# Performance work log

Measured on AMD Instinct MI355X. Metric: run time of the kernel, lower is better.

The kernel has to match this reference:

```python
import jax, jax.numpy as jnp
import numpy as np

N, K = 16384, 32          # num bboxes, context size
IN_F, HID = 608, 384      # in_features, hidden_dim
ALPHA = 0.2               # LeakyReLU slope
NEG_INF = -9e15


def setup_inputs() -> dict:
    key = jax.random.key(0)
    k1, k2, k3, k4, k5, k6, k7, k8 = jax.random.split(key, 8)
    h_i = jax.random.normal(k1, (N, IN_F), dtype=jnp.float32)
    idx = jax.random.randint(k2, (N, K), 0, N)
    pad = jax.random.uniform(k3, (N, K)) < 0.2
    context_indices = jnp.where(pad, -1, idx).astype(jnp.int64)
    s_in = 1.0 / np.sqrt(IN_F)
    s_a = 1.0 / np.sqrt(2 * HID)
    W_i = jax.random.uniform(k4, (IN_F, HID), minval=-s_in, maxval=s_in, dtype=jnp.float32)
    W_j = jax.random.uniform(k5, (IN_F, HID), minval=-s_in, maxval=s_in, dtype=jnp.float32)
    a_i = jax.random.uniform(k6, (HID,), minval=-s_a, maxval=s_a, dtype=jnp.float32)
    a_j = jax.random.uniform(k7, (HID,), minval=-s_a, maxval=s_a, dtype=jnp.float32)
    a_b = jax.random.uniform(k8, (1,), minval=-s_a, maxval=s_a, dtype=jnp.float32)
    return {"h_i": h_i, "context_indices": context_indices,
            "W_i": W_i, "W_j": W_j, "a_i": a_i, "a_j": a_j, "a_b": a_b}


def reference(h_i, context_indices, W_i, W_j, a_i, a_j, a_b):
    n = h_i.shape[0]
    Wh_i = h_i @ W_i                          # [N, H]
    # W_j has no bias, so projecting then gathering (zero pad row) equals
    # gathering zero-padded features then projecting.
    Wh_all = h_i @ W_j                        # [N, H]
    Wh_pad = jnp.concatenate([Wh_all, jnp.zeros((1, HID), Wh_all.dtype)], axis=0)
    idx = jnp.where(context_indices >= 0, context_indices, n)   # -1 -> zero row
    Wh_j = Wh_pad[idx]                        # [N, K, H] gather
    # attention_layer(concat(Wh_i, Wh_j)) == Wh_i@a_i + Wh_j@a_j + b
    scores = (Wh_i @ a_i)[:, None] + Wh_j @ a_j + a_b[0]        # [N, K]
    scores = jnp.where(scores > 0, scores, ALPHA * scores)      # LeakyReLU
    scores = jnp.where(context_indices >= 0, scores, NEG_INF)   # mask padding
    att = jax.nn.softmax(scores, axis=1)                        # [N, K]
    h_prime = jnp.einsum('nk,nkh->nh', att, Wh_j)               # [N, H]
    return h_prime
```

## Files before the change

kernel.cpp:

```cpp
#include <hip/hip_runtime.h>
#include <hip/hip_bf16.h>

typedef unsigned short u16;
typedef unsigned int u32;
typedef __attribute__((ext_vector_type(8))) __bf16 bf16x8;
typedef __attribute__((ext_vector_type(4))) float f32x4;

#define KCTX 32
#define INF_ 608
#define HID_ 384

#define WH_OFF 0
#define BT_OFF 12582912
#define V_OFF  13049856
#define SI_OFF 13052288
#define SJ_OFF 13117824
#define FL_OFF 13183360

__device__ __forceinline__ float bfu(u16 u)  { return __uint_as_float(((u32)u) << 16); }
__device__ __forceinline__ float bflo(u32 u) { return __uint_as_float(u << 16); }
__device__ __forceinline__ float bfhi(u32 u) { return __uint_as_float(u & 0xffff0000u); }
__device__ __forceinline__ u16 f2bf(float x) {
  u32 u = __float_as_uint(x);
  return (u16)((u + 0x7fffu + ((u >> 16) & 1u)) >> 16);
}
__device__ __forceinline__ void async_ld16(const void* g, void* l) {
  __builtin_amdgcn_global_load_lds(
      (const __attribute__((address_space(1))) u32*)g,
      (__attribute__((address_space(3))) u32*)l, 16, 0, 0);
}

__global__ __launch_bounds__(64) void detect_kernel(
    const u32* __restrict__ hw, const int* __restrict__ ci, int* __restrict__ flags) {
  const int lane = threadIdx.x;
  const u32 w = hw[lane];
  const int e = (int)((w >> 7) & 0xffu);
  const int bad = (e > 134 || e < 100) ? 1 : 0;
  const unsigned long long mb = __ballot(bad);
  const int hi = ci[2 * lane + 1];
  const int z = (hi == 0 || hi == -1) ? 1 : 0;
  const unsigned long long mz = __ballot(z);
  if (lane == 0) {
    flags[0] = (__popcll(mb) >= 16) ? 1 : 0;
    flags[1] = (__popcll(mz) >= 48) ? 1 : 0;
  }
}

__global__ __launch_bounds__(256) void prep_kernel(
    const void* __restrict__ Wi, const void* __restrict__ Wj,
    const void* __restrict__ ai, u16* __restrict__ Bt, float* __restrict__ v,
    const int* __restrict__ flags) {
  const int f32m = flags[0];
  const int t = blockIdx.x * 256 + threadIdx.x;
  const int hh = t / INF_;
  const int ff = t - hh * INF_;
  Bt[t] = f32m ? f2bf(((const float*)Wj)[ff * HID_ + hh])
               : ((const u16*)Wj)[ff * HID_ + hh];
  if (t < INF_) {
    float s = 0.f;
    if (f32m) {
      const float* wi = (const float*)Wi + (size_t)t * HID_;
      const float* a  = (const float*)ai;
      for (int c = 0; c < HID_; ++c) s += wi[c] * a[c];
    } else {
      const u16* wi = (const u16*)Wi + (size_t)t * HID_;
      const u16* a  = (const u16*)ai;
      for (int c = 0; c < HID_; ++c) s += bfu(wi[c]) * bfu(a[c]);
    }
    v[t] = s;
  }
}

__global__ __launch_bounds__(256, 2) void gemm_kernel(
    const void* __restrict__ A, const u16* __restrict__ Bt,
    u16* __restrict__ C, const int* __restrict__ flags) {
  __shared__ __align__(16) u16 As[128][32];
  __shared__ __align__(16) u16 Bs[128][32];
  const int f32m = flags[0];
  const int tid  = threadIdx.x;
  const int lane = tid & 63;
  const int wave = tid >> 6;
  const int row0 = blockIdx.x * 128;
  const int col0 = blockIdx.y * 128;
  const int wm = (wave & 1) * 64;
  const int wn = (wave >> 1) * 64;

  f32x4 acc[4][4];
#pragma unroll
  for (int i = 0; i < 4; ++i)
#pragma unroll
    for (int j = 0; j < 4; ++j) acc[i][j] = (f32x4){0.f, 0.f, 0.f, 0.f};

  const int c0 = tid, c1 = tid + 256;
  const int rA0 = c0 >> 2, kc0 = (c0 & 3) * 16;
  const int rA1 = c1 >> 2, kc1 = (c1 & 3) * 16;
  const char* Ab  = (const char*)A;
  const char* Btb = (const char*)Bt;

  for (int kt = 0; kt < 19; ++kt) {
    const size_t kb = (size_t)kt * 64;
    if (!f32m) {
      async_ld16(Ab + (size_t)(row0 + rA0) * 1216 + kb + kc0, (char*)As + c0 * 16);
      async_ld16(Ab + (size_t)(row0 + rA1) * 1216 + kb + kc1, (char*)As + c1 * 16);
    } else {
      const float* Af = (const float*)A;
#pragma unroll
      for (int j = 0; j < 4; ++j) {
        const int c = tid + j * 256;
        const int r = c >> 3, q = c & 7;
        const float4 fv = *(const float4*)(Af + (size_t)(row0 + r) * INF_ + kt * 32 + q * 4);
        ushort4 sv;
        sv.x = f2bf(fv.x); sv.y = f2bf(fv.y); sv.z = f2bf(fv.z); sv.w = f2bf(fv.w);
        *(ushort4*)&As[r][q * 4] = sv;
      }
    }
    async_ld16(Btb + (size_t)(col0 + rA0) * 1216 + kb + kc0, (char*)Bs + c0 * 16);
    async_ld16(Btb + (size_t)(col0 + rA1) * 1216 + kb + kc1, (char*)Bs + c1 * 16);
    __syncthreads();

    const int kk = (lane >> 4) * 8;
    const int lm = lane & 15;
    bf16x8 af[4], bfr[4];
#pragma unroll
    for (int i = 0; i < 4; ++i) af[i]  = *(const bf16x8*)&As[wm + i * 16 + lm][kk];
#pragma unroll
    for (int i = 0; i < 4; ++i) bfr[i] = *(const bf16x8*)&Bs[wn + i * 16 + lm][kk];
#pragma unroll
    for (int im = 0; im < 4; ++im)
#pragma unroll
      for (int in = 0; in < 4; ++in)
        acc[im][in] = __builtin_amdgcn_mfma_f32_16x16x32_bf16(
            af[im], bfr[in], acc[im][in], 0, 0, 0);
    __syncthreads();
  }

  const int lm = lane & 15, lq = lane >> 4;
#pragma unroll
  for (int im = 0; im < 4; ++im)
#pragma unroll
    for (int in = 0; in < 4; ++in) {
      const int colg = col0 + wn + in * 16 + lm;
#pragma unroll
      for (int r = 0; r < 4; ++r) {
        const int rowg = row0 + wm + im * 16 + lq * 4 + r;
        C[(size_t)rowg * HID_ + colg] = f2bf(acc[im][in][r]);
      }
    }
}

__global__ __launch_bounds__(256) void si_kernel(
    const void* __restrict__ h, const float* __restrict__ v,
    float* __restrict__ si, const int* __restrict__ flags) {
  const int f32m = flags[0];
  const int wave = threadIdx.x >> 6, lane = threadIdx.x & 63;
  const int n = blockIdx.x * 4 + wave;
  float sum = 0.f;
  if (f32m) {
    const float4* row = (const float4*)((const float*)h + (size_t)n * INF_);
    for (int c = lane; c < 152; c += 64) {
      float4 u = row[c];
      const float* vp = v + c * 4;
      sum += u.x * vp[0] + u.y * vp[1] + u.z * vp[2] + u.w * vp[3];
    }
  } else {
    const uint4* row = (const uint4*)((const u16*)h + (size_t)n * INF_);
    for (int c = lane; c < 76; c += 64) {
      uint4 u = row[c];
      const float* vp = v + c * 8;
      sum += bflo(u.x) * vp[0] + bfhi(u.x) * vp[1]
           + bflo(u.y) * vp[2] + bfhi(u.y) * vp[3]
           + bflo(u.z) * vp[4] + bfhi(u.z) * vp[5]
           + bflo(u.w) * vp[6] + bfhi(u.w) * vp[7];
    }
  }
#pragma unroll
  for (int o = 32; o; o >>= 1) sum += __shfl_down(sum, o);
  if (lane == 0) si[n] = sum;
}

__global__ __launch_bounds__(256) void sj_kernel(
    const u16* __restrict__ Wh, const void* __restrict__ aj,
    float* __restrict__ sj, const int* __restrict__ flags) {
  const int f32m = flags[0];
  const int wave = threadIdx.x >> 6, lane = threadIdx.x & 63;
  const int n = blockIdx.x * 4 + wave;
  const uint4* row = (const uint4*)(Wh + (size_t)n * HID_);
  float sum = 0.f;
  for (int c = lane; c < 48; c += 64) {
    uint4 u = row[c];
    float a0, a1, a2, a3, a4, a5, a6, a7;
    if (f32m) {
      const float* af = (const float*)aj + c * 8;
      a0 = af[0]; a1 = af[1]; a2 = af[2]; a3 = af[3];
      a4 = af[4]; a5 = af[5]; a6 = af[6]; a7 = af[7];
    } else {
      uint4 av = ((const uint4*)aj)[c];
      a0 = bflo(av.x); a1 = bfhi(av.x); a2 = bflo(av.y); a3 = bfhi(av.y);
      a4 = bflo(av.z); a5 = bfhi(av.z); a6 = bflo(av.w); a7 = bfhi(av.w);
    }
    sum += bflo(u.x) * a0 + bfhi(u.x) * a1 + bflo(u.y) * a2 + bfhi(u.y) * a3
         + bflo(u.z) * a4 + bfhi(u.z) * a5 + bflo(u.w) * a6 + bfhi(u.w) * a7;
  }
#pragma unroll
  for (int o = 32; o; o >>= 1) sum += __shfl_down(sum, o);
  if (lane == 0) sj[n] = sum;
}

__global__ __launch_bounds__(256) void attn_kernel(
    const int* __restrict__ ci, const float* __restrict__ si,
    const float* __restrict__ sj, const void* __restrict__ ab,
    const u16* __restrict__ Wh, void* __restrict__ out,
    const int* __restrict__ flags) {
  const int f32m = flags[0], i64 = flags[1];
  __shared__ float att_s[2][32];
  __shared__ int   idx_s[2][32];
  const int sub = threadIdx.x & 127;
  const int rb  = threadIdx.x >> 7;
  const int n   = blockIdx.x * 2 + rb;

  if (sub < 32) {
    const size_t t = (size_t)n * KCTX + sub;
    int idx;
    if (i64) { int lo = ci[2 * t], hi2 = ci[2 * t + 1]; idx = (hi2 < 0) ? -1 : lo; }
    else     { idx = ci[t]; }
    const bool valid = idx >= 0;
    const float sjv = valid ? sj[idx] : 0.f;
    const float bias = f32m ? ((const float*)ab)[0] : bfu(((const u16*)ab)[0]);
    float raw = si[n] + sjv + bias;
    float lr = raw > 0.f ? raw : 0.2f * raw;
    float s = valid ? lr : -9e15f;
    float m = s;
#pragma unroll
    for (int o = 16; o; o >>= 1) m = fmaxf(m, __shfl_xor(m, o));
    float p = expf(s - m);
    float d = p;
#pragma unroll
    for (int o = 16; o; o >>= 1) d += __shfl_xor(d, o);
    att_s[rb][sub] = valid ? p / d : 0.f;
    idx_s[rb][sub] = valid ? idx : 0;
  }
  __syncthreads();

  float a0 = 0.f, a1 = 0.f, a2 = 0.f;
#pragma unroll 4
  for (int k = 0; k < KCTX; ++k) {
    const float w = att_s[rb][k];
    const u16* row = Wh + (size_t)idx_s[rb][k] * HID_;
    a0 += w * bfu(row[sub]);
    a1 += w * bfu(row[sub + 128]);
    a2 += w * bfu(row[sub + 256]);
  }
  const size_t ob = (size_t)n * HID_;
  if (f32m) {
    float* o = (float*)out;
    o[ob + sub] = a0; o[ob + sub + 128] = a1; o[ob + sub + 256] = a2;
  } else {
    u16* o = (u16*)out;
    o[ob + sub] = f2bf(a0); o[ob + sub + 128] = f2bf(a1); o[ob + sub + 256] = f2bf(a2);
  }
}

extern "C" void kernel_launch(void* const* d_in, const int* in_sizes, int n_in,
                              void* d_out, int out_size, void* d_ws, size_t ws_size,
                              hipStream_t stream) {
  const void* h  = d_in[0];
  const int*  ci = (const int*)d_in[1];
  const void* Wi = d_in[2];
  const void* Wj = d_in[3];
  const void* ai = d_in[4];
  const void* aj = d_in[5];
  const void* ab = d_in[6];

  char* ws = (char*)d_ws;
  u16*   Wh = (u16*)(ws + WH_OFF);
  u16*   Bt = (u16*)(ws + BT_OFF);
  float* v  = (float*)(ws + V_OFF);
  float* si = (float*)(ws + SI_OFF);
  float* sj = (float*)(ws + SJ_OFF);
  int*   fl = (int*)(ws + FL_OFF);

  detect_kernel<<<1, 64, 0, stream>>>((const u32*)h, ci, fl);
  prep_kernel<<<912, 256, 0, stream>>>(Wi, Wj, ai, Bt, v, fl);
  dim3 g(128, 3);
  gemm_kernel<<<g, 256, 0, stream>>>(h, Bt, Wh, fl);
  si_kernel<<<4096, 256, 0, stream>>>(h, v, si, fl);
  sj_kernel<<<4096, 256, 0, stream>>>(Wh, aj, sj, fl);
  attn_kernel<<<8192, 256, 0, stream>>>(ci, si, sj, ab, Wh, d_out, fl);
}
```

Before: 185.1 us.

## Fuse detect/si/sj kernels into prep, GEMM epilogue and attention kernel

Removes the separate detect, si and sj kernels. Dtype detection is now done inline in each kernel. The s_j dot product is computed in the GEMM epilogue through shuffle reductions and atomicAdd, and s_i is computed inside the attention kernel. The prep kernel transposes W_j through a shared-memory tile and also zeroes sj. Attention now uses one wave per row with 16-byte gathers and __expf. This cuts three launches and the extra passes over Wh and h, at the cost of atomics and nondeterministic summation order in sj.

```diff
diff --git a/kernel.cpp b/kernel.cpp
--- a/kernel.cpp
+++ b/kernel.cpp
@@ -13,9 +13,7 @@
 #define WH_OFF 0
 #define BT_OFF 12582912
 #define V_OFF  13049856
-#define SI_OFF 13052288
-#define SJ_OFF 13117824
-#define FL_OFF 13183360
+#define SJ_OFF 13052288
 
 __device__ __forceinline__ float bfu(u16 u)  { return __uint_as_float(((u32)u) << 16); }
 __device__ __forceinline__ float bflo(u32 u) { return __uint_as_float(u << 16); }
@@ -30,53 +28,80 @@
       (__attribute__((address_space(3))) u32*)l, 16, 0, 0);
 }
 
-__global__ __launch_bounds__(64) void detect_kernel(
-    const u32* __restrict__ hw, const int* __restrict__ ci, int* __restrict__ flags) {
-  const int lane = threadIdx.x;
-  const u32 w = hw[lane];
+__device__ __forceinline__ int detect_f32(const u32* hw) {
+  const u32 w = hw[threadIdx.x & 63];
   const int e = (int)((w >> 7) & 0xffu);
-  const int bad = (e > 134 || e < 100) ? 1 : 0;
-  const unsigned long long mb = __ballot(bad);
-  const int hi = ci[2 * lane + 1];
-  const int z = (hi == 0 || hi == -1) ? 1 : 0;
-  const unsigned long long mz = __ballot(z);
-  if (lane == 0) {
-    flags[0] = (__popcll(mb) >= 16) ? 1 : 0;
-    flags[1] = (__popcll(mz) >= 48) ? 1 : 0;
-  }
+  const unsigned long long mb = __ballot(e > 134 || e < 100);
+  return __popcll(mb) >= 16;
+}
+__device__ __forceinline__ int detect_i64(const int* ci) {
+  const int hi = ci[2 * (threadIdx.x & 63) + 1];
+  const unsigned long long mz = __ballot(hi == 0 || hi == -1);
+  return __popcll(mz) >= 48;
 }
 
 __global__ __launch_bounds__(256) void prep_kernel(
-    const void* __restrict__ Wi, const void* __restrict__ Wj,
-    const void* __restrict__ ai, u16* __restrict__ Bt, float* __restrict__ v,
-    const int* __restrict__ flags) {
-  const int f32m = flags[0];
-  const int t = blockIdx.x * 256 + threadIdx.x;
-  const int hh = t / INF_;
-  const int ff = t - hh * INF_;
-  Bt[t] = f32m ? f2bf(((const float*)Wj)[ff * HID_ + hh])
-               : ((const u16*)Wj)[ff * HID_ + hh];
-  if (t < INF_) {
-    float s = 0.f;
-    if (f32m) {
-      const float* wi = (const float*)Wi + (size_t)t * HID_;
-      const float* a  = (const float*)ai;
-      for (int c = 0; c < HID_; ++c) s += wi[c] * a[c];
-    } else {
-      const u16* wi = (const u16*)Wi + (size_t)t * HID_;
-      const u16* a  = (const u16*)ai;
-      for (int c = 0; c < HID_; ++c) s += bfu(wi[c]) * bfu(a[c]);
-    }
-    v[t] = s;
+    const void* __restrict__ h, const void* __restrict__ Wi,
+    const void* __restrict__ Wj, const void* __restrict__ ai,
+    u16* __restrict__ Bt, float* __restrict__ v, float* __restrict__ sj) {
+  __shared__ u16 tile[64][65];
+  const int f32m = detect_f32((const u32*)h);
+  const int bid = blockIdx.x, tid = threadIdx.x;
+  if (bid < 60) {
+    const int ft = bid / 6, ht = bid - ft * 6;
+    const int f0 = ft * 64, h0 = ht * 64;
+    const int ln = tid & 63, fg = tid >> 6;
+#pragma unroll
+    for (int rr = 0; rr < 16; ++rr) {
+      const int fl = fg * 16 + rr;
+      const int f = f0 + fl;
+      if (f < INF_)
+        tile[fl][ln] = f32m ? f2bf(((const float*)Wj)[(size_t)f * HID_ + h0 + ln])
+                            : ((const u16*)Wj)[(size_t)f * HID_ + h0 + ln];
+    }
+    __syncthreads();
+#pragma unroll
+    for (int rr = 0; rr < 16; ++rr) {
+      const int hl = fg * 16 + rr;
+      const int f = f0 + ln;
+      if (f < INF_) Bt[(size_t)(h0 + hl) * INF_ + f] = tile[ln][hl];
+    }
+  } else if (bid < 63) {
+    const int t = (bid - 60) * 256 + tid;
+    if (t < INF_) {
+      float s = 0.f;
+      if (f32m) {
+        const float4* wi = (const float4*)((const float*)Wi + (size_t)t * HID_);
+        const float4* a4 = (const float4*)ai;
+        for (int c = 0; c < 96; ++c) {
+          float4 x = wi[c], y = a4[c];
+          s += x.x * y.x + x.y * y.y + x.z * y.z + x.w * y.w;
+        }
+      } else {
+        const uint4* wi = (const uint4*)((const u16*)Wi + (size_t)t * HID_);
+        const uint4* a4 = (const uint4*)ai;
+        for (int c = 0; c < 48; ++c) {
+          uint4 x = wi[c], y = a4[c];
+          s += bflo(x.x) * bflo(y.x) + bfhi(x.x) * bfhi(y.x)
+             + bflo(x.y) * bflo(y.y) + bfhi(x.y) * bfhi(y.y)
+             + bflo(x.z) * bflo(y.z) + bfhi(x.z) * bfhi(y.z)
+             + bflo(x.w) * bflo(y.w) + bfhi(x.w) * bfhi(y.w);
+        }
+      }
+      v[t] = s;
+    }
+  } else {
+#pragma unroll 8
+    for (int j = 0; j < 64; ++j) sj[j * 256 + tid] = 0.f;
   }
 }
 
 __global__ __launch_bounds__(256, 2) void gemm_kernel(
     const void* __restrict__ A, const u16* __restrict__ Bt,
-    u16* __restrict__ C, const int* __restrict__ flags) {
+    u16* __restrict__ C, const void* __restrict__ aj, float* __restrict__ sj) {
   __shared__ __align__(16) u16 As[128][32];
   __shared__ __align__(16) u16 Bs[128][32];
-  const int f32m = flags[0];
+  const int f32m = detect_f32((const u32*)A);
   const int tid  = threadIdx.x;
   const int lane = tid & 63;
   const int wave = tid >> 6;
@@ -119,12 +144,12 @@
     __syncthreads();
 
     const int kk = (lane >> 4) * 8;
-    const int lm = lane & 15;
+    const int lm0 = lane & 15;
     bf16x8 af[4], bfr[4];
 #pragma unroll
-    for (int i = 0; i < 4; ++i) af[i]  = *(const bf16x8*)&As[wm + i * 16 + lm][kk];
-#pragma unroll
-    for (int i = 0; i < 4; ++i) bfr[i] = *(const bf16x8*)&Bs[wn + i * 16 + lm][kk];
+    for (int i = 0; i < 4; ++i) af[i]  = *(const bf16x8*)&As[wm + i * 16 + lm0][kk];
+#pragma unroll
+    for (int i = 0; i < 4; ++i) bfr[i] = *(const bf16x8*)&Bs[wn + i * 16 + lm0][kk];
 #pragma unroll
     for (int im = 0; im < 4; ++im)
 #pragma unroll
@@ -146,117 +171,105 @@
         C[(size_t)rowg * HID_ + colg] = f2bf(acc[im][in][r]);
       }
     }
-}
-
-__global__ __launch_bounds__(256) void si_kernel(
-    const void* __restrict__ h, const float* __restrict__ v,
-    float* __restrict__ si, const int* __restrict__ flags) {
-  const int f32m = flags[0];
-  const int wave = threadIdx.x >> 6, lane = threadIdx.x & 63;
-  const int n = blockIdx.x * 4 + wave;
+  float ajv[4];
+#pragma unroll
+  for (int in = 0; in < 4; ++in) {
+    const int colg = col0 + wn + in * 16 + lm;
+    ajv[in] = f32m ? ((const float*)aj)[colg] : bfu(((const u16*)aj)[colg]);
+  }
+#pragma unroll
+  for (int im = 0; im < 4; ++im)
+#pragma unroll
+    for (int r = 0; r < 4; ++r) {
+      float p = acc[im][0][r] * ajv[0] + acc[im][1][r] * ajv[1]
+              + acc[im][2][r] * ajv[2] + acc[im][3][r] * ajv[3];
+      p += __shfl_xor(p, 1); p += __shfl_xor(p, 2);
+      p += __shfl_xor(p, 4); p += __shfl_xor(p, 8);
+      if (lm == 0) atomicAdd(&sj[row0 + wm + im * 16 + lq * 4 + r], p);
+    }
+}
+
+__global__ __launch_bounds__(256) void attn_kernel(
+    const void* __restrict__ h, const int* __restrict__ ci,
+    const float* __restrict__ v, const float* __restrict__ sj,
+    const void* __restrict__ ab, const u16* __restrict__ Wh,
+    void* __restrict__ out) {
+  __shared__ float att_s[4][32];
+  __shared__ int   idx_s[4][32];
+  const int f32m = detect_f32((const u32*)h);
+  const int i64  = detect_i64(ci);
+  const int wv = threadIdx.x >> 6;
+  const int lane = threadIdx.x & 63;
+  const int n = blockIdx.x * 4 + wv;
+
   float sum = 0.f;
   if (f32m) {
-    const float4* row = (const float4*)((const float*)h + (size_t)n * INF_);
+    const float4* hrow = (const float4*)((const float*)h + (size_t)n * INF_);
+    const float4* v4 = (const float4*)v;
     for (int c = lane; c < 152; c += 64) {
-      float4 u = row[c];
-      const float* vp = v + c * 4;
-      sum += u.x * vp[0] + u.y * vp[1] + u.z * vp[2] + u.w * vp[3];
+      float4 u = hrow[c], w = v4[c];
+      sum += u.x * w.x + u.y * w.y + u.z * w.z + u.w * w.w;
     }
   } else {
-    const uint4* row = (const uint4*)((const u16*)h + (size_t)n * INF_);
+    const uint4* hrow = (const uint4*)((const u16*)h + (size_t)n * INF_);
+    const float4* v4 = (const float4*)v;
     for (int c = lane; c < 76; c += 64) {
-      uint4 u = row[c];
-      const float* vp = v + c * 8;
-      sum += bflo(u.x) * vp[0] + bfhi(u.x) * vp[1]
-           + bflo(u.y) * vp[2] + bfhi(u.y) * vp[3]
-           + bflo(u.z) * vp[4] + bfhi(u.z) * vp[5]
-           + bflo(u.w) * vp[6] + bfhi(u.w) * vp[7];
-    }
-  }
-#pragma unroll
-  for (int o = 32; o; o >>= 1) sum += __shfl_down(sum, o);
-  if (lane == 0) si[n] = sum;
-}
-
-__global__ __launch_bounds__(256) void sj_kernel(
-    const u16* __restrict__ Wh, const void* __restrict__ aj,
-    float* __restrict__ sj, const int* __restrict__ flags) {
-  const int f32m = flags[0];
-  const int wave = threadIdx.x >> 6, lane = threadIdx.x & 63;
-  const int n = blockIdx.x * 4 + wave;
-  const uint4* row = (const uint4*)(Wh + (size_t)n * HID_);
-  float sum = 0.f;
-  for (int c = lane; c < 48; c += 64) {
-    uint4 u = row[c];
-    float a0, a1, a2, a3, a4, a5, a6, a7;
-    if (f32m) {
-      const float* af = (const float*)aj + c * 8;
-      a0 = af[0]; a1 = af[1]; a2 = af[2]; a3 = af[3];
-      a4 = af[4]; a5 = af[5]; a6 = af[6]; a7 = af[7];
-    } else {
-      uint4 av = ((const uint4*)aj)[c];
-      a0 = bflo(av.x); a1 = bfhi(av.x); a2 = bflo(av.y); a3 = bfhi(av.y);
-      a4 = bflo(av.z); a5 = bfhi(av.z); a6 = bflo(av.w); a7 = bfhi(av.w);
-    }
-    sum += bflo(u.x) * a0 + bfhi(u.x) * a1 + bflo(u.y) * a2 + bfhi(u.y) * a3
-         + bflo(u.z) * a4 + bfhi(u.z) * a5 + bflo(u.w) * a6 + bfhi(u.w) * a7;
-  }
-#pragma unroll
-  for (int o = 32; o; o >>= 1) sum += __shfl_down(sum, o);
-  if (lane == 0) sj[n] = sum;
-}
-
-__global__ __launch_bounds__(256) void attn_kernel(
-    const int* __restrict__ ci, const float* __restrict__ si,
-    const float* __restrict__ sj, const void* __restrict__ ab,
-    const u16* __restrict__ Wh, void* __restrict__ out,
-    const int* __restrict__ flags) {
-  const int f32m = flags[0], i64 = flags[1];
-  __shared__ float att_s[2][32];
-  __shared__ int   idx_s[2][32];
-  const int sub = threadIdx.x & 127;
-  const int rb  = threadIdx.x >> 7;
-  const int n   = blockIdx.x * 2 + rb;
-
-  if (sub < 32) {
-    const size_t t = (size_t)n * KCTX + sub;
+      uint4 u = hrow[c];
+      float4 w0 = v4[2 * c], w1 = v4[2 * c + 1];
+      sum += bflo(u.x) * w0.x + bfhi(u.x) * w0.y + bflo(u.y) * w0.z + bfhi(u.y) * w0.w
+           + bflo(u.z) * w1.x + bfhi(u.z) * w1.y + bflo(u.w) * w1.z + bfhi(u.w) * w1.w;
+    }
+  }
+#pragma unroll
+  for (int o = 32; o; o >>= 1) sum += __shfl_xor(sum, o);
+
+  if (lane < 32) {
+    const size_t t = (size_t)n * KCTX + lane;
     int idx;
-    if (i64) { int lo = ci[2 * t], hi2 = ci[2 * t + 1]; idx = (hi2 < 0) ? -1 : lo; }
+    if (i64) { int lo = ci[2 * t], hi = ci[2 * t + 1]; idx = (hi < 0) ? -1 : lo; }
     else     { idx = ci[t]; }
     const bool valid = idx >= 0;
     const float sjv = valid ? sj[idx] : 0.f;
     const float bias = f32m ? ((const float*)ab)[0] : bfu(((const u16*)ab)[0]);
-    float raw = si[n] + sjv + bias;
+    float raw = sum + sjv + bias;
     float lr = raw > 0.f ? raw : 0.2f * raw;
     float s = valid ? lr : -9e15f;
     float m = s;
 #pragma unroll
-    for (int o = 16; o; o >>= 1) m = fmaxf(m, __shfl_xor(m, o));
-    float p = expf(s - m);
+    for (int o = 16; o; o >>= 1) m = fmaxf(m, __shfl_xor(m, o, 32));
+    float p = __expf(s - m);
     float d = p;
 #pragma unroll
-    for (int o = 16; o; o >>= 1) d += __shfl_xor(d, o);
-    att_s[rb][sub] = valid ? p / d : 0.f;
-    idx_s[rb][sub] = valid ? idx : 0;
+    for (int o = 16; o; o >>= 1) d += __shfl_xor(d, o, 32);
+    att_s[wv][lane] = valid ? p / d : 0.f;
+    idx_s[wv][lane] = valid ? idx : 0;
   }
   __syncthreads();
 
-  float a0 = 0.f, a1 = 0.f, a2 = 0.f;
+  if (lane < 48) {
+    float a0 = 0, a1 = 0, a2 = 0, a3 = 0, a4 = 0, a5 = 0, a6 = 0, a7 = 0;
 #pragma unroll 4
-  for (int k = 0; k < KCTX; ++k) {
-    const float w = att_s[rb][k];
-    const u16* row = Wh + (size_t)idx_s[rb][k] * HID_;
-    a0 += w * bfu(row[sub]);
-    a1 += w * bfu(row[sub + 128]);
-    a2 += w * bfu(row[sub + 256]);
-  }
-  const size_t ob = (size_t)n * HID_;
-  if (f32m) {
-    float* o = (float*)out;
-    o[ob + sub] = a0; o[ob + sub + 128] = a1; o[ob + sub + 256] = a2;
-  } else {
-    u16* o = (u16*)out;
-    o[ob + sub] = f2bf(a0); o[ob + sub + 128] = f2bf(a1); o[ob + sub + 256] = f2bf(a2);
+    for (int k = 0; k < KCTX; ++k) {
+      const float w = att_s[wv][k];
+      const uint4* row = (const uint4*)(Wh + (u32)idx_s[wv][k] * HID_);
+      const uint4 q = row[lane];
+      a0 += w * bflo(q.x); a1 += w * bfhi(q.x);
+      a2 += w * bflo(q.y); a3 += w * bfhi(q.y);
+      a4 += w * bflo(q.z); a5 += w * bfhi(q.z);
+      a6 += w * bflo(q.w); a7 += w * bfhi(q.w);
+    }
+    if (f32m) {
+      float4* o4 = (float4*)out + (size_t)n * 96 + lane * 2;
+      o4[0] = (float4){a0, a1, a2, a3};
+      o4[1] = (float4){a4, a5, a6, a7};
+    } else {
+      uint4 o;
+      o.x = (u32)f2bf(a0) | ((u32)f2bf(a1) << 16);
+      o.y = (u32)f2bf(a2) | ((u32)f2bf(a3) << 16);
+      o.z = (u32)f2bf(a4) | ((u32)f2bf(a5) << 16);
+      o.w = (u32)f2bf(a6) | ((u32)f2bf(a7) << 16);
+      ((uint4*)out)[(size_t)n * 48 + lane] = o;
+    }
   }
 }
 
@@ -267,23 +280,18 @@
   const int*  ci = (const int*)d_in[1];
   const void* Wi = d_in[2];
   const void* Wj = d_in[3];
+  const void* aj = d_in[5];
   const void* ai = d_in[4];
-  const void* aj = d_in[5];
   const void* ab = d_in[6];
 
   char* ws = (char*)d_ws;
   u16*   Wh = (u16*)(ws + WH_OFF);
   u16*   Bt = (u16*)(ws + BT_OFF);
   float* v  = (float*)(ws + V_OFF);
-  float* si = (float*)(ws + SI_OFF);
   float* sj = (float*)(ws + SJ_OFF);
-  int*   fl = (int*)(ws + FL_OFF);
-
-  detect_kernel<<<1, 64, 0, stream>>>((const u32*)h, ci, fl);
-  prep_kernel<<<912, 256, 0, stream>>>(Wi, Wj, ai, Bt, v, fl);
+
+  prep_kernel<<<64, 256, 0, stream>>>(h, Wi, Wj, ai, Bt, v, sj);
   dim3 g(128, 3);
-  gemm_kernel<<<g, 256, 0, stream>>>(h, Bt, Wh, fl);
-  si_kernel<<<4096, 256, 0, stream>>>(h, v, si, fl);
-  sj_kernel<<<4096, 256, 0, stream>>>(Wh, aj, sj, fl);
-  attn_kernel<<<8192, 256, 0, stream>>>(ci, si, sj, ab, Wh, d_out, fl);
-}
+  gemm_kernel<<<g, 256, 0, stream>>>(h, Bt, Wh, aj, sj);
+  attn_kernel<<<4096, 256, 0, stream>>>(h, ci, v, sj, ab, Wh, d_out);
+}
```

Result: faster. 176.9 us (-4.5%).
